# Performance work log

Measured on AMD Instinct MI355X. Metric: run time of the kernel, lower is better.

The kernel has to match this reference:

```python
import jax, jax.numpy as jnp
import numpy as np

B, S, D, H = 2, 2048, 1024, 16
DK = D // H


def setup_inputs() -> dict:
    key = jax.random.key(0)
    ks = jax.random.split(key, 9)
    w_scale = 1.0 / np.sqrt(D)  # xavier-ish scale
    return {
        "q": jax.random.normal(ks[0], (B, S, D), dtype=jnp.float32),
        "k": jax.random.normal(ks[1], (B, S, D), dtype=jnp.float32),
        "v": jax.random.normal(ks[2], (B, S, D), dtype=jnp.float32),
        "A": jax.random.uniform(ks[3], (S, S), dtype=jnp.float32),
        "Wq": jax.random.normal(ks[4], (D, D), dtype=jnp.float32) * w_scale,
        "bq": jnp.zeros((D,), jnp.float32),
        "Wk": jax.random.normal(ks[5], (D, D), dtype=jnp.float32) * w_scale,
        "bk": jnp.zeros((D,), jnp.float32),
        "Wv": jax.random.normal(ks[6], (D, D), dtype=jnp.float32) * w_scale,
        "bv": jnp.zeros((D,), jnp.float32),
        "Wo": jax.random.normal(ks[7], (D, D), dtype=jnp.float32) * w_scale,
        "bo": jnp.zeros((D,), jnp.float32),
    }


def _proj(x, W, b):
    # nn.Linear: x @ W^T + b, then split heads -> [B, H, S, DK]
    y = jnp.einsum("bsd,ed->bse", x, W) + b
    return y.reshape(B, S, H, DK).transpose(0, 2, 1, 3)


def reference(q, k, v, A, Wq, bq, Wk, bk, Wv, bv, Wo, bo):
    qh = _proj(q, Wq, bq)  # [B,H,S,DK]
    kh = _proj(k, Wk, bk)
    vh = _proj(v, Wv, bv)
    scale = 1.0 / jnp.sqrt(jnp.asarray(DK, qh.dtype))
    scores = jnp.einsum("bhqd,bhkd->bhqk", qh, kh) * scale  # [B,H,S,S]
    # No softmax: scores multiplied by structural mask A^T (dropout disabled, eval)
    p_attn = scores * A.T
    x = jnp.einsum("bhqk,bhkd->bhqd", p_attn, vh)
    x = x.transpose(0, 2, 1, 3).reshape(B, S, D)
    return jnp.einsum("bsd,ed->bse", x, Wo) + bo
```

## Files before the change

kernel.cpp:

```cpp
#include <hip/hip_runtime.h>

#define SEQ    2048
#define DMODEL 1024
#define NHEAD  16
#define DHEAD  64
#define NBATCH 2

typedef __bf16 bf16x8 __attribute__((ext_vector_type(8)));
typedef float f32x16 __attribute__((ext_vector_type(16)));
typedef float f32x8 __attribute__((ext_vector_type(8)));
typedef unsigned short ushort8v __attribute__((ext_vector_type(8)));
typedef unsigned int uint2v __attribute__((ext_vector_type(2)));
typedef int int4v __attribute__((ext_vector_type(4)));

static __device__ __forceinline__ unsigned short f2b(float f){
  unsigned int u = __builtin_bit_cast(unsigned int, f);
  u += 0x7fffu + ((u>>16)&1u);
  return (unsigned short)(u>>16);
}
static __device__ __forceinline__ float b2f(unsigned short h){
  unsigned int u = ((unsigned int)h)<<16;
  return __builtin_bit_cast(float, u);
}
static __device__ __forceinline__ f32x16 mfma32(bf16x8 a, bf16x8 b, f32x16 c){
  return __builtin_amdgcn_mfma_f32_32x32x16_bf16(a,b,c,0,0,0);
}
static __device__ __forceinline__ ushort8v cvt8(const float* p){
  float4 f0 = *(const float4*)p;
  float4 f1 = *(const float4*)(p+4);
  ushort8v r;
  r[0]=f2b(f0.x); r[1]=f2b(f0.y); r[2]=f2b(f0.z); r[3]=f2b(f0.w);
  r[4]=f2b(f1.x); r[5]=f2b(f1.y); r[6]=f2b(f1.z); r[7]=f2b(f1.w);
  return r;
}

__global__ __launch_bounds__(256) void cvtXpack(
    const float* __restrict__ q, const float* __restrict__ k, const float* __restrict__ v,
    unsigned short* __restrict__ Xq, unsigned short* __restrict__ Xk, unsigned short* __restrict__ Xv)
{
  const int z = blockIdx.z;
  const float* S = (z==0)? q : (z==1)? k : v;
  unsigned short* D = (z==0)? Xq : (z==1)? Xk : Xv;
  const int g = blockIdx.x;
  const int wave = threadIdx.x>>6, lane = threadIdx.x&63;
  const int l31 = lane&31, hi = lane>>5;
  const float* src = S + (size_t)(g*32 + l31)*DMODEL + 8*hi + 256*wave;
  unsigned short* dst = D + (size_t)(g*64 + wave*16)*512 + lane*8;
  #pragma unroll
  for (int i=0;i<16;i++)
    *(ushort8v*)(dst + (size_t)i*512) = cvt8(src + 16*i);
}

__global__ __launch_bounds__(256) void cvtWpack(
    const float* __restrict__ Wq, const float* __restrict__ Wk,
    const float* __restrict__ Wv, const float* __restrict__ Wo,
    unsigned short* __restrict__ Wp)
{
  const int z = blockIdx.z;
  const float* S = (z==0)? Wq : (z==1)? Wk : (z==2)? Wv : Wo;
  const int g = blockIdx.x;
  const int wave = threadIdx.x>>6, lane = threadIdx.x&63;
  const int l31 = lane&31, hi = lane>>5;
  const float* src = S + (size_t)(g*32 + l31)*DMODEL + 8*hi + 256*wave;
  unsigned short* dst = Wp + (size_t)((z*32 + g)*64 + wave*16)*512 + lane*8;
  #pragma unroll
  for (int i=0;i<16;i++)
    *(ushort8v*)(dst + (size_t)i*512) = cvt8(src + 16*i);
}

__global__ __launch_bounds__(256) void cvtA(const float* __restrict__ A,
                                            unsigned short* __restrict__ Am){
  const int tid  = threadIdx.x;
  const int lane = tid&63, l31 = lane&31, hi = lane>>5;
  const int q32  = blockIdx.x;
  const int kt   = blockIdx.y*4 + (tid>>6);
  const int q    = q32*32 + l31;

  unsigned short out8[4][8];
  #pragma unroll
  for (int fi=0; fi<2; fi++){
    #pragma unroll
    for (int mm=0; mm<4; mm++){
      #pragma unroll
      for (int j=0; j<4; j++){
        const int k = kt*64 + 32*fi + 8*mm + 4*hi + j;
        out8[fi*2 + (mm>>1)][(mm&1)*4 + j] = f2b(A[(size_t)k*SEQ + q]);
      }
    }
  }
  unsigned short* dst = Am + ((size_t)(q32*32 + kt)*4)*512 + lane*8;
  #pragma unroll
  for (int w=0; w<4; w++)
    *(ushort8v*)(dst + (size_t)w*512) = *(const ushort8v*)out8[w];
}

__global__ __launch_bounds__(256,3) void proj_qkv(
    const unsigned short* __restrict__ Xq, const unsigned short* __restrict__ Xk, const unsigned short* __restrict__ Xv,
    const unsigned short* __restrict__ Wp,
    const float* __restrict__ bq, const float* __restrict__ bk, const float* __restrict__ bv,
    unsigned short* __restrict__ qh, unsigned short* __restrict__ Kp, unsigned short* __restrict__ Vp)
{
  const int z = blockIdx.z;
  const unsigned short* X = (z==0)? Xq : (z==1)? Xk : Xv;
  const unsigned short* W = Wp + (size_t)z*1048576;
  const float* bias = (z==0)? bq : (z==1)? bk : bv;
  const float alpha = (z==0)? 0.125f : 1.0f;

  const int orig = blockIdx.y*8 + blockIdx.x;
  const int virt = (orig&7)*32 + (orig>>3);
  const int bx = virt&7, by = virt>>3;
  const int mb = by*128, nb = bx*128;

  const int tid = threadIdx.x;
  const int lane = tid&63, wave = tid>>6;
  const int wr = wave>>1, wc = wave&1, l31 = lane&31, hi = lane>>5;
  f32x16 acc[2][2] = {};

  const unsigned short* a0p = X + (size_t)((mb>>5) + 2*wr)*32768 + lane*8;
  const unsigned short* a1p = a0p + 32768;
  const unsigned short* b0p = W + (size_t)((nb>>5) + 2*wc)*32768 + lane*8;
  const unsigned short* b1p = b0p + 32768;

  #pragma unroll 4
  for (int s=0;s<64;s++){
    bf16x8 a0 = *(const bf16x8*)(a0p + (size_t)s*512);
    bf16x8 a1 = *(const bf16x8*)(a1p + (size_t)s*512);
    bf16x8 b0 = *(const bf16x8*)(b0p + (size_t)s*512);
    bf16x8 b1 = *(const bf16x8*)(b1p + (size_t)s*512);
    acc[0][0] = mfma32(a0,b0,acc[0][0]);
    acc[0][1] = mfma32(a0,b1,acc[0][1]);
    acc[1][0] = mfma32(a1,b0,acc[1][0]);
    acc[1][1] = mfma32(a1,b1,acc[1][1]);
  }

  #pragma unroll
  for (int fj=0; fj<2; fj++){
    const int e = nb + 64*wc + 32*fj + l31;
    const float bv_ = bias[e];
    const int hh = e>>6, dk = e&63;
    #pragma unroll
    for (int fi=0; fi<2; fi++){
      #pragma unroll
      for (int r=0;r<16;r++){
        const int i = mb + 64*wr + 32*fi + (r&3) + 8*(r>>2) + 4*hi;
        const int bb = i>>11, ss = i&(SEQ-1);
        const int bhh = bb*NHEAD + hh;
        const unsigned short val = f2b((acc[fi][fj][r] + bv_)*alpha);
        if (z==0){
          qh[((size_t)bhh*SEQ + ss)*DHEAD + dk] = val;
        } else if (z==1){
          const size_t addr = (((size_t)(bhh*64 + (ss>>5))*4 + (dk>>4))*64
                               + ((dk>>3)&1)*32 + (ss&31))*8 + (dk&7);
          Kp[addr] = val;
        } else {
          const size_t addr = ((((size_t)(bhh*32 + (ss>>6))*4 + ((ss>>4)&3))*2
                               + (dk>>5))*64 + ((ss>>3)&1)*32 + (dk&31))*8 + (ss&7);
          Vp[addr] = val;
        }
      }
    }
  }
}

__global__ __launch_bounds__(512,2) void attn(
    const unsigned short* __restrict__ qh, const unsigned short* __restrict__ Kp,
    const unsigned short* __restrict__ Vp, const unsigned short* __restrict__ Am,
    unsigned short* __restrict__ xp)
{
  const int orig = blockIdx.y*16 + blockIdx.x;
  const int xcd = orig&7, within = orig>>3;
  const int bh   = xcd*4 + (within>>4);
  const int qblk = within&15;

  const int tid  = threadIdx.x;
  const int lane = tid&63, wave = tid>>6;
  const int qsub = wave&3, khalf = wave>>2;
  const int l31 = lane&31, hi = lane>>5;

  const int q32  = qblk*4 + qsub;
  const int qrow = q32*32 + l31;
  const unsigned short* qp = qh + ((size_t)bh*SEQ + qrow)*DHEAD;
  bf16x8 Qf[4];
  #pragma unroll
  for (int t=0;t<4;t++) Qf[t] = *(const bf16x8*)(qp + 16*t + 8*hi);

  f32x16 xacc[2] = {};

  const unsigned short* kpb = Kp + ((size_t)bh*64)*2048 + lane*8;
  const unsigned short* vpb = Vp + ((size_t)bh*32)*4096 + lane*8;
  const unsigned short* apb = Am + ((size_t)q32*32)*2048 + lane*8;

  bf16x8 Ka[8], Kb[8];
  ushort8v Aa[4], Ab[4];

  #define LOADK(DST, KT) { \
    const unsigned short* _kp = kpb + (size_t)((KT)*2)*2048; \
    _Pragma("unroll") \
    for (int s=0;s<8;s++) DST[s] = *(const bf16x8*)(_kp + (size_t)s*512); }
  #define LOADA(DST, KT) { \
    const unsigned short* _ap = apb + (size_t)(KT)*2048; \
    _Pragma("unroll") \
    for (int w=0;w<4;w++) DST[w] = *(const ushort8v*)(_ap + (size_t)w*512); }

  LOADK(Ka, khalf*16);
  LOADA(Aa, khalf*16);

  #define BODY(T, KR, AR, KN, AN, TN) { \
    const int _kt = khalf*16 + (T); \
    const unsigned short* _vp = vpb + (size_t)_kt*4096; \
    bf16x8 Vr[8]; \
    _Pragma("unroll") \
    for (int s=0;s<8;s++) Vr[s] = *(const bf16x8*)(_vp + (size_t)s*512); \
    LOADK(KN, khalf*16 + (TN)); \
    LOADA(AN, khalf*16 + (TN)); \
    unsigned int wv[2][4], xv[2][4]; \
    _Pragma("unroll") \
    for (int fi=0; fi<2; fi++){ \
      f32x16 sacc = {}; \
      _Pragma("unroll") \
      for (int s=0;s<4;s++) \
        sacc = mfma32(KR[fi*4+s], Qf[s], sacc); \
      ushort8v a80 = AR[fi*2+0], a81 = AR[fi*2+1]; \
      _Pragma("unroll") \
      for (int mm=0; mm<4; mm++){ \
        const int b0 = (mm&1)*4, rb2 = 4*mm; \
        float p0 = sacc[rb2+0]*((mm>>1)? b2f(a81[b0+0]) : b2f(a80[b0+0])); \
        float p1 = sacc[rb2+1]*((mm>>1)? b2f(a81[b0+1]) : b2f(a80[b0+1])); \
        float p2 = sacc[rb2+2]*((mm>>1)? b2f(a81[b0+2]) : b2f(a80[b0+2])); \
        float p3 = sacc[rb2+3]*((mm>>1)? b2f(a81[b0+3]) : b2f(a80[b0+3])); \
        asm("v_cvt_pk_bf16_f32 %0, %1, %2" : "=v"(wv[fi][mm]) : "v"(p0), "v"(p1)); \
        asm("v_cvt_pk_bf16_f32 %0, %1, %2" : "=v"(xv[fi][mm]) : "v"(p2), "v"(p3)); \
      } \
    } \
    __builtin_amdgcn_s_setprio(1); \
    _Pragma("unroll") \
    for (int s2=0; s2<4; s2++){ \
      const int fi = s2>>1, sl = s2&1; \
      uint2v rw = __builtin_amdgcn_permlane32_swap(wv[fi][2*sl], wv[fi][2*sl+1], false, false); \
      uint2v rx = __builtin_amdgcn_permlane32_swap(xv[fi][2*sl], xv[fi][2*sl+1], false, false); \
      int4v av; av.x = (int)rw[0]; av.y = (int)rx[0]; av.z = (int)rw[1]; av.w = (int)rx[1]; \
      bf16x8 pa = __builtin_bit_cast(bf16x8, av); \
      xacc[0] = mfma32(pa, Vr[s2*2+0], xacc[0]); \
      xacc[1] = mfma32(pa, Vr[s2*2+1], xacc[1]); \
    } \
    __builtin_amdgcn_s_setprio(0); }

  #pragma unroll 1
  for (int tt=0; tt<8; tt++){
    const int t0 = 2*tt, t1 = 2*tt+1;
    BODY(t0, Ka, Aa, Kb, Ab, t1);
    BODY(t1, Kb, Ab, Ka, Aa, (t1+1)&15);
  }
  #undef BODY
  #undef LOADK
  #undef LOADA

  __shared__ float Red[4][64][33];
  if (khalf==1){
    #pragma unroll
    for (int j=0;j<2;j++)
      #pragma unroll
      for (int r=0;r<16;r++)
        Red[qsub][lane][16*j+r] = xacc[j][r];
  }
  __syncthreads();
  if (khalf==0){
    #pragma unroll
    for (int j=0;j<2;j++)
      #pragma unroll
      for (int r=0;r<16;r++)
        xacc[j][r] += Red[qsub][lane][16*j+r];
    const int b = bh>>4, h = bh&15;
    #pragma unroll
    for (int fj=0; fj<2; fj++){
      const int scol = h*4 + fj*2 + (l31>>4);
      const int lpart = ((l31>>3)&1)*32;
      const int epart = l31&7;
      #pragma unroll
      for (int r=0;r<16;r++){
        const int qq = q32*32 + (r&3) + 8*(r>>2) + 4*hi;
        const int row = b*SEQ + qq;
        const size_t addr = ((size_t)(row>>5)*64 + scol)*512 + (lpart + (row&31))*8 + epart;
        xp[addr] = f2b(xacc[fj][r]);
      }
    }
  }
}

__global__ __launch_bounds__(256,4) void oproj(
    const unsigned short* __restrict__ Xp, const unsigned short* __restrict__ Wop,
    const float* __restrict__ bo, float* __restrict__ out)
{
  const int orig = blockIdx.y*16 + blockIdx.x;
  const int virt = (orig&7)*64 + (orig>>3);
  const int bx = virt&15, by = virt>>4;
  const int mb = by*128, nb = bx*64;

  const int tid = threadIdx.x;
  const int lane = tid&63, wave = tid>>6;
  const int l31 = lane&31, hi = lane>>5;
  f32x16 acc[2] = {};

  const unsigned short* ap  = Xp  + (size_t)((mb>>5) + wave)*32768 + lane*8;
  const unsigned short* b0p = Wop + (size_t)(nb>>5)*32768 + lane*8;
  const unsigned short* b1p = b0p + 32768;

  #pragma unroll 4
  for (int s=0;s<64;s++){
    bf16x8 a  = *(const bf16x8*)(ap  + (size_t)s*512);
    bf16x8 b0 = *(const bf16x8*)(b0p + (size_t)s*512);
    bf16x8 b1 = *(const bf16x8*)(b1p + (size_t)s*512);
    acc[0] = mfma32(a,b0,acc[0]);
    acc[1] = mfma32(a,b1,acc[1]);
  }

  #pragma unroll
  for (int fj=0; fj<2; fj++){
    const int e = nb + 32*fj + l31;
    const float bv_ = bo[e];
    #pragma unroll
    for (int r=0;r<16;r++){
      const int i = mb + 32*wave + (r&3) + 8*(r>>2) + 4*hi;
      out[(size_t)i*DMODEL + e] = acc[fj][r] + bv_;
    }
  }
}

extern "C" void kernel_launch(void* const* d_in, const int* in_sizes, int n_in,
                              void* d_out, int out_size, void* d_ws, size_t ws_size,
                              hipStream_t stream)
{
  const float* q  = (const float*)d_in[0];
  const float* k  = (const float*)d_in[1];
  const float* v  = (const float*)d_in[2];
  const float* A  = (const float*)d_in[3];
  const float* Wq = (const float*)d_in[4];
  const float* bq = (const float*)d_in[5];
  const float* Wk = (const float*)d_in[6];
  const float* bk = (const float*)d_in[7];
  const float* Wv = (const float*)d_in[8];
  const float* bv = (const float*)d_in[9];
  const float* Wo = (const float*)d_in[10];
  const float* bo = (const float*)d_in[11];
  float* out = (float*)d_out;

  unsigned short* ws = (unsigned short*)d_ws;
  const size_t NE = (size_t)NBATCH*SEQ*DMODEL;
  unsigned short* qh  = ws;
  unsigned short* Kp  = qh + NE;
  unsigned short* Vp  = Kp + NE;
  unsigned short* xb  = Vp + NE;
  unsigned short* Wp  = xb + NE;
  unsigned short* Xqp = (unsigned short*)d_out;
  unsigned short* Xkp = Xqp + NE;
  unsigned short* Am  = (unsigned short*)d_out;
  unsigned short* Xvp = xb;

  cvtXpack<<<dim3(128, 1, 3), 256, 0, stream>>>(q, k, v, Xqp, Xkp, Xvp);
  cvtWpack<<<dim3(32, 1, 4), 256, 0, stream>>>(Wq, Wk, Wv, Wo, Wp);
  proj_qkv<<<dim3(8, 32, 3), 256, 0, stream>>>(
      Xqp, Xkp, Xvp, Wp, bq, bk, bv, qh, Kp, Vp);
  cvtA<<<dim3(64, 8), 256, 0, stream>>>(A, Am);
  attn<<<dim3(16, 32), 512, 0, stream>>>(qh, Kp, Vp, Am, xb);
  oproj<<<dim3(16, 32), 256, 0, stream>>>(xb, Wp + (size_t)3*1048576, bo, out);
}
```

Measured before the change: 142.0 us.

## Double-buffer GEMM register loads and halve attention block size

The projection and output GEMM inner loops now use explicit two-stage register double buffering with unroll 1, so the next step's global loads are issued before the current step's MFMAs. The attention kernel goes from 512-thread blocks covering 4 query tiles to 256-thread blocks covering 2, which doubles the grid and adjusts the XCD mapping and the reduction buffer. The aim is better latency hiding and finer scheduling granularity. The cost is possibly less reuse of K, V and A loads per block, and the compiler may already have pipelined the unrolled loops.

```diff
diff --git a/kernel.cpp b/kernel.cpp
--- a/kernel.cpp
+++ b/kernel.cpp
@@ -121,17 +121,27 @@
   const unsigned short* b0p = W + (size_t)((nb>>5) + 2*wc)*32768 + lane*8;
   const unsigned short* b1p = b0p + 32768;
 
-  #pragma unroll 4
-  for (int s=0;s<64;s++){
-    bf16x8 a0 = *(const bf16x8*)(a0p + (size_t)s*512);
-    bf16x8 a1 = *(const bf16x8*)(a1p + (size_t)s*512);
-    bf16x8 b0 = *(const bf16x8*)(b0p + (size_t)s*512);
-    bf16x8 b1 = *(const bf16x8*)(b1p + (size_t)s*512);
-    acc[0][0] = mfma32(a0,b0,acc[0][0]);
-    acc[0][1] = mfma32(a0,b1,acc[0][1]);
-    acc[1][0] = mfma32(a1,b0,acc[1][0]);
-    acc[1][1] = mfma32(a1,b1,acc[1][1]);
-  }
+  bf16x8 Ca[4], Cb[4];
+  #define LDP(D,S) { \
+    D[0] = *(const bf16x8*)(a0p + (size_t)(S)*512); \
+    D[1] = *(const bf16x8*)(a1p + (size_t)(S)*512); \
+    D[2] = *(const bf16x8*)(b0p + (size_t)(S)*512); \
+    D[3] = *(const bf16x8*)(b1p + (size_t)(S)*512); }
+  LDP(Ca,0)
+  #pragma unroll 1
+  for (int s=0; s<64; s+=2){
+    LDP(Cb, s+1)
+    acc[0][0] = mfma32(Ca[0],Ca[2],acc[0][0]);
+    acc[0][1] = mfma32(Ca[0],Ca[3],acc[0][1]);
+    acc[1][0] = mfma32(Ca[1],Ca[2],acc[1][0]);
+    acc[1][1] = mfma32(Ca[1],Ca[3],acc[1][1]);
+    LDP(Ca, (s+2)&63)
+    acc[0][0] = mfma32(Cb[0],Cb[2],acc[0][0]);
+    acc[0][1] = mfma32(Cb[0],Cb[3],acc[0][1]);
+    acc[1][0] = mfma32(Cb[1],Cb[2],acc[1][0]);
+    acc[1][1] = mfma32(Cb[1],Cb[3],acc[1][1]);
+  }
+  #undef LDP
 
   #pragma unroll
   for (int fj=0; fj<2; fj++){
@@ -162,22 +172,22 @@
   }
 }
 
-__global__ __launch_bounds__(512,2) void attn(
+__global__ __launch_bounds__(256,4) void attn(
     const unsigned short* __restrict__ qh, const unsigned short* __restrict__ Kp,
     const unsigned short* __restrict__ Vp, const unsigned short* __restrict__ Am,
     unsigned short* __restrict__ xp)
 {
-  const int orig = blockIdx.y*16 + blockIdx.x;
+  const int orig = blockIdx.y*32 + blockIdx.x;
   const int xcd = orig&7, within = orig>>3;
-  const int bh   = xcd*4 + (within>>4);
-  const int qblk = within&15;
+  const int bh   = xcd*4 + (within>>5);
+  const int qblk = within&31;
 
   const int tid  = threadIdx.x;
   const int lane = tid&63, wave = tid>>6;
-  const int qsub = wave&3, khalf = wave>>2;
+  const int qsub = wave&1, khalf = wave>>1;
   const int l31 = lane&31, hi = lane>>5;
 
-  const int q32  = qblk*4 + qsub;
+  const int q32  = qblk*2 + qsub;
   const int qrow = q32*32 + l31;
   const unsigned short* qp = qh + ((size_t)bh*SEQ + qrow)*DHEAD;
   bf16x8 Qf[4];
@@ -255,7 +265,7 @@
   #undef LOADK
   #undef LOADA
 
-  __shared__ float Red[4][64][33];
+  __shared__ float Red[2][64][33];
   if (khalf==1){
     #pragma unroll
     for (int j=0;j<2;j++)
@@ -305,14 +315,22 @@
   const unsigned short* b0p = Wop + (size_t)(nb>>5)*32768 + lane*8;
   const unsigned short* b1p = b0p + 32768;
 
-  #pragma unroll 4
-  for (int s=0;s<64;s++){
-    bf16x8 a  = *(const bf16x8*)(ap  + (size_t)s*512);
-    bf16x8 b0 = *(const bf16x8*)(b0p + (size_t)s*512);
-    bf16x8 b1 = *(const bf16x8*)(b1p + (size_t)s*512);
-    acc[0] = mfma32(a,b0,acc[0]);
-    acc[1] = mfma32(a,b1,acc[1]);
-  }
+  bf16x8 Ca[3], Cb[3];
+  #define LDO(D,S) { \
+    D[0] = *(const bf16x8*)(ap  + (size_t)(S)*512); \
+    D[1] = *(const bf16x8*)(b0p + (size_t)(S)*512); \
+    D[2] = *(const bf16x8*)(b1p + (size_t)(S)*512); }
+  LDO(Ca,0)
+  #pragma unroll 1
+  for (int s=0; s<64; s+=2){
+    LDO(Cb, s+1)
+    acc[0] = mfma32(Ca[0],Ca[1],acc[0]);
+    acc[1] = mfma32(Ca[0],Ca[2],acc[1]);
+    LDO(Ca, (s+2)&63)
+    acc[0] = mfma32(Cb[0],Cb[1],acc[0]);
+    acc[1] = mfma32(Cb[0],Cb[2],acc[1]);
+  }
+  #undef LDO
 
   #pragma unroll
   for (int fj=0; fj<2; fj++){
@@ -361,6 +379,6 @@
   proj_qkv<<<dim3(8, 32, 3), 256, 0, stream>>>(
       Xqp, Xkp, Xvp, Wp, bq, bk, bv, qh, Kp, Vp);
   cvtA<<<dim3(64, 8), 256, 0, stream>>>(A, Am);
-  attn<<<dim3(16, 32), 512, 0, stream>>>(qh, Kp, Vp, Am, xb);
+  attn<<<dim3(32, 32), 256, 0, stream>>>(qh, Kp, Vp, Am, xb);
   oproj<<<dim3(16, 32), 256, 0, stream>>>(xb, Wp + (size_t)3*1048576, bo, out);
 }
```

After: 318.6 us. +124.3%, slower.

## Share K/V tiles via LDS double buffering instead of split-K waves

Applied to the files above, without the earlier changes.

The attention kernel moves from 512-thread blocks, where two wave groups split the key range and reduce through shared memory, to 256-thread blocks in which four waves each own a query sub-block and walk all 32 key tiles. K and V tiles are staged cooperatively into double-buffered LDS with global_load_lds, so each tile is fetched from global memory once per block rather than once per wave. This removes the cross-wave reduction and the redundant per-wave K/V global loads. In exchange it adds a block barrier every iteration and LDS read traffic, and each wave now runs a serial loop twice as long.

```diff
diff --git a/kernel.cpp b/kernel.cpp
--- a/kernel.cpp
+++ b/kernel.cpp
@@ -33,6 +33,9 @@
   r[4]=f2b(f1.x); r[5]=f2b(f1.y); r[6]=f2b(f1.z); r[7]=f2b(f1.w);
   return r;
 }
+#define GLOAD16(g,l) __builtin_amdgcn_global_load_lds( \
+    (const __attribute__((address_space(1))) void*)(g), \
+    (__attribute__((address_space(3))) void*)(l), 16, 0, 0)
 
 __global__ __launch_bounds__(256) void cvtXpack(
     const float* __restrict__ q, const float* __restrict__ k, const float* __restrict__ v,
@@ -162,7 +165,7 @@
   }
 }
 
-__global__ __launch_bounds__(512,2) void attn(
+__global__ __launch_bounds__(256,2) void attn(
     const unsigned short* __restrict__ qh, const unsigned short* __restrict__ Kp,
     const unsigned short* __restrict__ Vp, const unsigned short* __restrict__ Am,
     unsigned short* __restrict__ xp)
@@ -174,10 +177,9 @@
 
   const int tid  = threadIdx.x;
   const int lane = tid&63, wave = tid>>6;
-  const int qsub = wave&3, khalf = wave>>2;
   const int l31 = lane&31, hi = lane>>5;
 
-  const int q32  = qblk*4 + qsub;
+  const int q32  = qblk*4 + wave;
   const int qrow = q32*32 + l31;
   const unsigned short* qp = qh + ((size_t)bh*SEQ + qrow)*DHEAD;
   bf16x8 Qf[4];
@@ -186,40 +188,44 @@
 
   f32x16 xacc[2] = {};
 
-  const unsigned short* kpb = Kp + ((size_t)bh*64)*2048 + lane*8;
-  const unsigned short* vpb = Vp + ((size_t)bh*32)*4096 + lane*8;
-  const unsigned short* apb = Am + ((size_t)q32*32)*2048 + lane*8;
-
-  bf16x8 Ka[8], Kb[8];
+  const unsigned short* kpb = Kp + (size_t)bh*131072 + lane*8;
+  const unsigned short* vpb = Vp + (size_t)bh*131072 + lane*8;
+  const unsigned short* apb = Am + (size_t)q32*65536 + lane*8;
+
+  __shared__ unsigned short Klds[2][4096];
+  __shared__ unsigned short Vlds[2][4096];
+
   ushort8v Aa[4], Ab[4];
 
-  #define LOADK(DST, KT) { \
-    const unsigned short* _kp = kpb + (size_t)((KT)*2)*2048; \
-    _Pragma("unroll") \
-    for (int s=0;s<8;s++) DST[s] = *(const bf16x8*)(_kp + (size_t)s*512); }
+  #define STAGE(BUF, KT) { \
+    const unsigned short* _k = kpb + (size_t)(KT)*4096; \
+    const unsigned short* _v = vpb + (size_t)(KT)*4096; \
+    GLOAD16(_k + (size_t)(2*wave  )*512, &Klds[BUF][(2*wave  )*512]); \
+    GLOAD16(_k + (size_t)(2*wave+1)*512, &Klds[BUF][(2*wave+1)*512]); \
+    GLOAD16(_v + (size_t)(2*wave  )*512, &Vlds[BUF][(2*wave  )*512]); \
+    GLOAD16(_v + (size_t)(2*wave+1)*512, &Vlds[BUF][(2*wave+1)*512]); }
+
   #define LOADA(DST, KT) { \
     const unsigned short* _ap = apb + (size_t)(KT)*2048; \
     _Pragma("unroll") \
     for (int w=0;w<4;w++) DST[w] = *(const ushort8v*)(_ap + (size_t)w*512); }
 
-  LOADK(Ka, khalf*16);
-  LOADA(Aa, khalf*16);
-
-  #define BODY(T, KR, AR, KN, AN, TN) { \
-    const int _kt = khalf*16 + (T); \
-    const unsigned short* _vp = vpb + (size_t)_kt*4096; \
-    bf16x8 Vr[8]; \
-    _Pragma("unroll") \
-    for (int s=0;s<8;s++) Vr[s] = *(const bf16x8*)(_vp + (size_t)s*512); \
-    LOADK(KN, khalf*16 + (TN)); \
-    LOADA(AN, khalf*16 + (TN)); \
+  STAGE(0, 0);
+  LOADA(Aa, 0);
+  __syncthreads();
+
+  #define BODY(KT, BUF, AR, AN) { \
+    STAGE((BUF)^1, ((KT)+1)&31); \
+    LOADA(AN, ((KT)+1)&31); \
     unsigned int wv[2][4], xv[2][4]; \
     _Pragma("unroll") \
     for (int fi=0; fi<2; fi++){ \
       f32x16 sacc = {}; \
       _Pragma("unroll") \
-      for (int s=0;s<4;s++) \
-        sacc = mfma32(KR[fi*4+s], Qf[s], sacc); \
+      for (int s=0;s<4;s++){ \
+        bf16x8 kf = *(const bf16x8*)&Klds[BUF][(fi*4+s)*512 + lane*8]; \
+        sacc = mfma32(kf, Qf[s], sacc); \
+      } \
       ushort8v a80 = AR[fi*2+0], a81 = AR[fi*2+1]; \
       _Pragma("unroll") \
       for (int mm=0; mm<4; mm++){ \
@@ -240,49 +246,35 @@
       uint2v rx = __builtin_amdgcn_permlane32_swap(xv[fi][2*sl], xv[fi][2*sl+1], false, false); \
       int4v av; av.x = (int)rw[0]; av.y = (int)rx[0]; av.z = (int)rw[1]; av.w = (int)rx[1]; \
       bf16x8 pa = __builtin_bit_cast(bf16x8, av); \
-      xacc[0] = mfma32(pa, Vr[s2*2+0], xacc[0]); \
-      xacc[1] = mfma32(pa, Vr[s2*2+1], xacc[1]); \
+      bf16x8 v0 = *(const bf16x8*)&Vlds[BUF][(s2*2+0)*512 + lane*8]; \
+      bf16x8 v1 = *(const bf16x8*)&Vlds[BUF][(s2*2+1)*512 + lane*8]; \
+      xacc[0] = mfma32(pa, v0, xacc[0]); \
+      xacc[1] = mfma32(pa, v1, xacc[1]); \
     } \
-    __builtin_amdgcn_s_setprio(0); }
+    __builtin_amdgcn_s_setprio(0); \
+    __syncthreads(); }
 
   #pragma unroll 1
-  for (int tt=0; tt<8; tt++){
-    const int t0 = 2*tt, t1 = 2*tt+1;
-    BODY(t0, Ka, Aa, Kb, Ab, t1);
-    BODY(t1, Kb, Ab, Ka, Aa, (t1+1)&15);
+  for (int tt=0; tt<16; tt++){
+    BODY(2*tt,   0, Aa, Ab);
+    BODY(2*tt+1, 1, Ab, Aa);
   }
   #undef BODY
-  #undef LOADK
+  #undef STAGE
   #undef LOADA
 
-  __shared__ float Red[4][64][33];
-  if (khalf==1){
+  const int b = bh>>4, h = bh&15;
+  #pragma unroll
+  for (int fj=0; fj<2; fj++){
+    const int scol = h*4 + fj*2 + (l31>>4);
+    const int lpart = ((l31>>3)&1)*32;
+    const int epart = l31&7;
     #pragma unroll
-    for (int j=0;j<2;j++)
-      #pragma unroll
-      for (int r=0;r<16;r++)
-        Red[qsub][lane][16*j+r] = xacc[j][r];
-  }
-  __syncthreads();
-  if (khalf==0){
-    #pragma unroll
-    for (int j=0;j<2;j++)
-      #pragma unroll
-      for (int r=0;r<16;r++)
-        xacc[j][r] += Red[qsub][lane][16*j+r];
-    const int b = bh>>4, h = bh&15;
-    #pragma unroll
-    for (int fj=0; fj<2; fj++){
-      const int scol = h*4 + fj*2 + (l31>>4);
-      const int lpart = ((l31>>3)&1)*32;
-      const int epart = l31&7;
-      #pragma unroll
-      for (int r=0;r<16;r++){
-        const int qq = q32*32 + (r&3) + 8*(r>>2) + 4*hi;
-        const int row = b*SEQ + qq;
-        const size_t addr = ((size_t)(row>>5)*64 + scol)*512 + (lpart + (row&31))*8 + epart;
-        xp[addr] = f2b(xacc[fj][r]);
-      }
+    for (int r=0;r<16;r++){
+      const int qq = q32*32 + (r&3) + 8*(r>>2) + 4*hi;
+      const int row = b*SEQ + qq;
+      const size_t addr = ((size_t)(row>>5)*64 + scol)*512 + (lpart + (row&31))*8 + epart;
+      xp[addr] = f2b(xacc[fj][r]);
     }
   }
 }
@@ -361,6 +353,6 @@
   proj_qkv<<<dim3(8, 32, 3), 256, 0, stream>>>(
       Xqp, Xkp, Xvp, Wp, bq, bk, bv, qh, Kp, Vp);
   cvtA<<<dim3(64, 8), 256, 0, stream>>>(A, Am);
-  attn<<<dim3(16, 32), 512, 0, stream>>>(qh, Kp, Vp, Am, xb);
+  attn<<<dim3(16, 32), 256, 0, stream>>>(qh, Kp, Vp, Am, xb);
   oproj<<<dim3(16, 32), 256, 0, stream>>>(xb, Wp + (size_t)3*1048576, bo, out);
 }
```

Result: faster. 133.7 us (-5.8%).
